# Kernel optimization log

Hardware: AMD Instinct MI355X
Metric: run time of the kernel (lower is better)

## Reference

```python
import jax, jax.numpy as jnp
import numpy as np

B, P, K = 8, 1024, 20          # clouds, points per cloud, knn neighbors
H, HD = 256, 512               # module hidden_dim, edge-MLP hidden (TransformerBlockRes default)
L, C = 3, 512                  # n_hidden_layers, n_components
N = B * P
LN_EPS = 1e-5


def _layer_norm(x, g, b):
    m = jnp.mean(x, axis=-1, keepdims=True)
    v = jnp.var(x, axis=-1, keepdims=True)
    return (x - m) * jax.lax.rsqrt(v + LN_EPS) * g + b


def _mlp(x, W1, b1, g1, be1, W2, b2, g2, be2):
    # Linear -> LayerNorm -> ELU -> Linear -> LayerNorm -> ELU (pos_nn / attn_nn)
    h = jax.nn.elu(_layer_norm(x @ W1 + b1, g1, be1))
    return jax.nn.elu(_layer_norm(h @ W2 + b2, g2, be2))


def _knn(pos):
    # knn_graph within each cloud, loop=False (self excluded). Equal-size clouds.
    p = pos.reshape(B, P, 3)
    d2 = jnp.sum((p[:, :, None, :] - p[:, None, :, :]) ** 2, axis=-1)  # [B,P,P]
    d2 = d2 + jnp.eye(P, dtype=d2.dtype) * 1e10                        # exclude self
    idx = jax.lax.top_k(-d2, K)[1]                                     # [B,P,K]
    return (idx + (jnp.arange(B) * P)[:, None, None]).reshape(N, K)    # global ids


def setup_inputs() -> dict:
    key = jax.random.key(0)
    cnt = [0]

    def nrm(shape, scale):
        cnt[0] += 1
        return (jax.random.normal(jax.random.fold_in(key, cnt[0]), shape, dtype=jnp.float32) * scale)

    d = {}
    d["pos"] = nrm((N, 3), 1.0)
    d["batch"] = jnp.repeat(jnp.arange(B, dtype=jnp.int32), P)
    # stem Linear(3, H)
    d["ffm_W"] = nrm((3, H), 3 ** -0.5); d["ffm_b"] = jnp.zeros((H,), jnp.float32)
    # PointTransformerConv linears (no bias), stacked over L layers
    s = H ** -0.5
    d["lin_W"] = nrm((L, H, H), s); d["src_W"] = nrm((L, H, H), s); d["dst_W"] = nrm((L, H, H), s)
    # pos_nn: Linear(3,HD)+LN+ELU+Linear(HD,H)+LN+ELU
    d["pos1_W"] = nrm((L, 3, HD), 3 ** -0.5); d["pos1_b"] = jnp.zeros((L, HD), jnp.float32)
    d["pos_ln1_g"] = jnp.ones((L, HD), jnp.float32); d["pos_ln1_b"] = jnp.zeros((L, HD), jnp.float32)
    d["pos2_W"] = nrm((L, HD, H), HD ** -0.5); d["pos2_b"] = jnp.zeros((L, H), jnp.float32)
    d["pos_ln2_g"] = jnp.ones((L, H), jnp.float32); d["pos_ln2_b"] = jnp.zeros((L, H), jnp.float32)
    # attn_nn: Linear(H,HD)+LN+ELU+Linear(HD,H)+LN+ELU
    d["att1_W"] = nrm((L, H, HD), s); d["att1_b"] = jnp.zeros((L, HD), jnp.float32)
    d["att_ln1_g"] = jnp.ones((L, HD), jnp.float32); d["att_ln1_b"] = jnp.zeros((L, HD), jnp.float32)
    d["att2_W"] = nrm((L, HD, H), HD ** -0.5); d["att2_b"] = jnp.zeros((L, H), jnp.float32)
    d["att_ln2_g"] = jnp.ones((L, H), jnp.float32); d["att_ln2_b"] = jnp.zeros((L, H), jnp.float32)
    # per-layer tail: LayerNorm + ELU + Linear + ResidualCoefficient
    d["blk_ln_g"] = jnp.ones((L, H), jnp.float32); d["blk_ln_b"] = jnp.zeros((L, H), jnp.float32)
    d["blk_W"] = nrm((L, H, H), s); d["blk_b"] = jnp.zeros((L, H), jnp.float32)
    d["res_alpha"] = nrm((L,), 0.1)  # torch init is zeros; small random for a nontrivial test
    d["r1_W"] = nrm((H, H), s); d["r1_b"] = jnp.zeros((H,), jnp.float32)
    d["r2_W"] = nrm((H, H), s); d["r2_b"] = jnp.zeros((H,), jnp.float32)
    d["r2_ln_g"] = jnp.ones((H,), jnp.float32); d["r2_ln_b"] = jnp.zeros((H,), jnp.float32)
    d["r3_W"] = nrm((H, H), s); d["r3_b"] = jnp.zeros((H,), jnp.float32)
    d["r3_ln_g"] = jnp.ones((H,), jnp.float32); d["r3_ln_b"] = jnp.zeros((H,), jnp.float32)
    d["r4_W"] = nrm((H, C), s); d["r4_b"] = jnp.zeros((C,), jnp.float32)
    return d


def reference(pos, batch, ffm_W, ffm_b, lin_W, src_W, dst_W,
              pos1_W, pos1_b, pos_ln1_g, pos_ln1_b, pos2_W, pos2_b, pos_ln2_g, pos_ln2_b,
              att1_W, att1_b, att_ln1_g, att_ln1_b, att2_W, att2_b, att_ln2_g, att_ln2_b,
              blk_ln_g, blk_ln_b, blk_W, blk_b, res_alpha,
              r1_W, r1_b, r2_W, r2_b, r2_ln_g, r2_ln_b, r3_W, r3_b, r3_ln_g, r3_ln_b, r4_W, r4_b):
    # knn graph is identical every layer (pos never changes) -> compute once
    neigh = _knn(pos)                       # [N,K] neighbor (source) ids j for each target i
    rel = pos[:, None, :] - pos[neigh]      # pos_i - pos_j, [N,K,3]
    x = pos @ ffm_W + ffm_b                 # [N,H]
    for i in range(L):
        a_src = x @ src_W[i]                # [N,H]
        a_dst = x @ dst_W[i]
        v = x @ lin_W[i]
        delta = _mlp(rel, pos1_W[i], pos1_b[i], pos_ln1_g[i], pos_ln1_b[i],
                     pos2_W[i], pos2_b[i], pos_ln2_g[i], pos_ln2_b[i])          # [N,K,H]
        alpha = _mlp(a_dst[:, None, :] - a_src[neigh] + delta,
                     att1_W[i], att1_b[i], att_ln1_g[i], att_ln1_b[i],
                     att2_W[i], att2_b[i], att_ln2_g[i], att_ln2_b[i])          # [N,K,H]
        attn = jax.nn.softmax(alpha, axis=1)                                    # per-channel over K neighbors
        agg = jnp.sum(attn * (v[neigh] + delta), axis=1)                        # sum aggregation (PyG default)
        h = jax.nn.elu(_layer_norm(agg, blk_ln_g[i], blk_ln_b[i])) @ blk_W[i] + blk_b[i]
        x = x + res_alpha[i] * h
    h = x @ r1_W + r1_b                                                         # [N,H]
    pooled = jax.ops.segment_max(h, batch, num_segments=B)                      # global_max_pool [B,H]
    h = jax.nn.elu(_layer_norm(pooled @ r2_W + r2_b, r2_ln_g, r2_ln_b))
    h = jax.nn.elu(_layer_norm(h @ r3_W + r3_b, r3_ln_g, r3_ln_b))
    return h @ r4_W + r4_b                                                      # [B,C]
```

## Files before the change

### kernel.cpp

```cpp
#include <hip/hip_runtime.h>
#include <math.h>

#define NPTS 8192
#define PPC  1024
#define BCL  8
#define KNN  20
#define HDIM 256
#define HD2  512
#define NL   3
#define NCOMP 512
#define EDG  (NPTS*KNN)
#define QS   768

typedef __bf16 bf16x8 __attribute__((ext_vector_type(8)));
typedef float f32x4 __attribute__((ext_vector_type(4)));
typedef unsigned int uint4v __attribute__((ext_vector_type(4)));
typedef unsigned short us8 __attribute__((ext_vector_type(8)));

__device__ inline unsigned short f2bf(float f) {
  unsigned u = __float_as_uint(f);
  u += 0x7FFF + ((u >> 16) & 1);
  return (unsigned short)(u >> 16);
}
__device__ inline unsigned short f2bf_fast(float f) {
  return (unsigned short)((__float_as_uint(f) + 0x8000u) >> 16);
}
__device__ inline unsigned pack2bf(float a, float b) {
  return ((__float_as_uint(a) + 0x8000u) >> 16) |
         ((__float_as_uint(b) + 0x8000u) & 0xFFFF0000u);
}
__device__ inline float bf2f(unsigned short u) {
  return __uint_as_float((unsigned)u << 16);
}
__device__ inline float elu(float y) { return (y > 0.f) ? y : (__expf(y) - 1.f); }

__global__ __launch_bounds__(256)
void knn_wave(const float* __restrict__ pos, int* __restrict__ neigh,
              float* __restrict__ rel_f) {
  __shared__ float px[PPC], py[PPC], pz[PPC];
  int tid = threadIdx.x;
  int i0 = blockIdx.x * 4;
  int base = i0 & ~(PPC - 1);
  for (int t = tid; t < PPC; t += 256) {
    px[t] = pos[(size_t)(base + t) * 3 + 0];
    py[t] = pos[(size_t)(base + t) * 3 + 1];
    pz[t] = pos[(size_t)(base + t) * 3 + 2];
  }
  __syncthreads();
  int wave = tid >> 6, lane = tid & 63;
  int i = i0 + wave;
  int il = i - base;
  float xi = px[il], yi = py[il], zi = pz[il];
  float d[16];
  #pragma unroll
  for (int q = 0; q < 16; ++q) {
    int t = lane + 64 * q;
    float dx = xi - px[t], dy = yi - py[t], dz = zi - pz[t];
    float dd = dx * dx + dy * dy + dz * dz;
    d[q] = (t == il) ? 3.4e38f : dd;
  }
  int mywin = 0;
  for (int k = 0; k < KNN; ++k) {
    float v = d[0]; int idx = lane;
    #pragma unroll
    for (int q = 1; q < 16; ++q)
      if (d[q] < v) { v = d[q]; idx = q * 64 + lane; }
    #pragma unroll
    for (int off = 1; off < 64; off <<= 1) {
      float ov = __shfl_xor(v, off, 64);
      int oi = __shfl_xor(idx, off, 64);
      if (ov < v || (ov == v && oi < idx)) { v = ov; idx = oi; }
    }
    if (lane == k) mywin = idx;
    int qwin = idx >> 6;
    bool own = (idx & 63) == lane;
    #pragma unroll
    for (int q = 0; q < 16; ++q)
      if (own && q == qwin) d[q] = 3.4e38f;
  }
  if (lane < KNN) {
    neigh[(size_t)i * KNN + lane] = base + mywin;
    size_t rb = ((size_t)i * KNN + lane) * 3;
    rel_f[rb + 0] = xi - px[mywin];
    rel_f[rb + 1] = yi - py[mywin];
    rel_f[rb + 2] = zi - pz[mywin];
  }
}

__global__ __launch_bounds__(256)
void transpose_w(const float* __restrict__ W, unsigned short* __restrict__ out,
                 int K, int N, int Kpad) {
  int n = blockIdx.x;
  for (int k = threadIdx.x; k < Kpad; k += 256)
    out[(size_t)n * Kpad + k] = (k < K) ? f2bf(W[(size_t)k * N + n]) : (unsigned short)0;
}

__global__ __launch_bounds__(64)
void pack_w(const float* __restrict__ W, unsigned short* __restrict__ out, int N) {
  int blk = blockIdx.x;
  int NT = N / 16;
  int ks = blk / NT, nt = blk % NT;
  int lane = threadIdx.x;
  int l16 = lane & 15, quad = lane >> 4;
  int col = nt * 16 + l16;
  int krow = ks * 32 + quad * 8;
  unsigned short o[8];
  #pragma unroll
  for (int j = 0; j < 8; ++j)
    o[j] = f2bf(W[(size_t)(krow + j) * N + col]);
  *(uint4v*)&out[((size_t)blk * 64 + lane) * 8] = *(uint4v*)o;
}

__global__ __launch_bounds__(256)
void prep_pos(const float* __restrict__ pos, unsigned short* __restrict__ posb) {
  int idx = blockIdx.x * 256 + threadIdx.x;
  int m = idx >> 5, c = idx & 31;
  posb[idx] = (c < 3) ? f2bf(pos[(size_t)m * 3 + c]) : (unsigned short)0;
}

__global__ __launch_bounds__(256, 3)
void pos_fused(const float* __restrict__ rel_f, const float* __restrict__ W1,
               const float* __restrict__ b1, const float* __restrict__ g1,
               const float* __restrict__ be1,
               const unsigned short* __restrict__ B2p, const float* __restrict__ bias2,
               const float* __restrict__ g2, const float* __restrict__ be2,
               unsigned short* __restrict__ delta_b, int edge_base) {
  __shared__ alignas(16) char smem[46976];
  unsigned short* H = (unsigned short*)smem;
  float* w1s = (float*)(smem + 33280);
  float* b1s = w1s + 1536;
  float* g1s = b1s + 512;
  float* be1s = g1s + 512;
  float* lnsum = (float*)(smem + 45568);
  float* lnsq  = (float*)(smem + 46080);
  float* relS  = (float*)(smem + 46592);
  int tid = threadIdx.x;
  int wave = tid >> 6, lane = tid & 63;
  int el0 = blockIdx.x * 32;
  int eg0 = edge_base + el0;
  for (int t = tid; t < 1536; t += 256) w1s[t] = W1[t];
  for (int t = tid; t < 512; t += 256) { b1s[t] = b1[t]; g1s[t] = g1[t]; be1s[t] = be1[t]; }
  if (tid < 96) relS[tid] = rel_f[(size_t)eg0 * 3 + tid];
  __syncthreads();
  {
    int rIW = lane >> 3, sub = lane & 7;
    int row = wave * 8 + rIW;
    float r0 = relS[row * 3 + 0], r1v = relS[row * 3 + 1], r2v = relS[row * 3 + 2];
    int cb = sub * 64;
    float h[64]; float s = 0.f, sq = 0.f;
    #pragma unroll
    for (int cc = 0; cc < 16; ++cc) {
      f32x4 w0 = *(const f32x4*)&w1s[cb + cc * 4];
      f32x4 wa = *(const f32x4*)&w1s[512 + cb + cc * 4];
      f32x4 wb = *(const f32x4*)&w1s[1024 + cb + cc * 4];
      f32x4 bb = *(const f32x4*)&b1s[cb + cc * 4];
      #pragma unroll
      for (int q = 0; q < 4; ++q) {
        float hv = fmaf(r0, w0[q], fmaf(r1v, wa[q], fmaf(r2v, wb[q], bb[q])));
        h[cc * 4 + q] = hv; s += hv; sq += hv * hv;
      }
    }
    #pragma unroll
    for (int off = 1; off < 8; off <<= 1) { s += __shfl_xor(s, off, 64); sq += __shfl_xor(sq, off, 64); }
    float mean = s * (1.f / 512.f);
    float var = sq * (1.f / 512.f) - mean * mean;
    float rr = rsqrtf(var + 1e-5f);
    #pragma unroll
    for (int cc = 0; cc < 8; ++cc) {
      unsigned u[4];
      #pragma unroll
      for (int q = 0; q < 4; ++q) {
        int c0 = cb + cc * 8 + 2 * q;
        float y0 = elu((h[cc * 8 + 2 * q]     - mean) * rr * g1s[c0]     + be1s[c0]);
        float y1 = elu((h[cc * 8 + 2 * q + 1] - mean) * rr * g1s[c0 + 1] + be1s[c0 + 1]);
        u[q] = pack2bf(y0, y1);
      }
      *(uint4v*)&H[row * 520 + cb + cc * 8] = *(uint4v*)u;
    }
  }
  __syncthreads();
  int quad = lane >> 4, l16 = lane & 15;
  int cb2 = wave * 64;
  f32x4 acc2[2][4] = {};
  #pragma unroll 4
  for (int ks = 0; ks < 16; ++ks) {
    bf16x8 bvv[4];
    #pragma unroll
    for (int ni = 0; ni < 4; ++ni)
      bvv[ni] = *(const bf16x8*)(B2p + ((size_t)(ks * 16 + wave * 4 + ni) * 64 + lane) * 8);
    bf16x8 a0 = __builtin_bit_cast(bf16x8, *(const uint4v*)&H[(l16) * 520 + ks * 32 + quad * 8]);
    bf16x8 a1 = __builtin_bit_cast(bf16x8, *(const uint4v*)&H[(16 + l16) * 520 + ks * 32 + quad * 8]);
    #pragma unroll
    for (int ni = 0; ni < 4; ++ni) {
      acc2[0][ni] = __builtin_amdgcn_mfma_f32_16x16x32_bf16(a0, bvv[ni], acc2[0][ni], 0, 0, 0);
      acc2[1][ni] = __builtin_amdgcn_mfma_f32_16x16x32_bf16(a1, bvv[ni], acc2[1][ni], 0, 0, 0);
    }
  }
  float b2v[4], g2v[4], be2v[4];
  #pragma unroll
  for (int ni = 0; ni < 4; ++ni) {
    int col = cb2 + ni * 16 + l16;
    b2v[ni] = bias2[col]; g2v[ni] = g2[col]; be2v[ni] = be2[col];
  }
  #pragma unroll
  for (int mt = 0; mt < 2; ++mt)
    #pragma unroll
    for (int r = 0; r < 4; ++r) {
      int row = mt * 16 + quad * 4 + r;
      float s2 = 0.f, q2 = 0.f;
      #pragma unroll
      for (int ni = 0; ni < 4; ++ni) {
        float val = acc2[mt][ni][r] + b2v[ni];
        acc2[mt][ni][r] = val; s2 += val; q2 += val * val;
      }
      #pragma unroll
      for (int off = 1; off < 16; off <<= 1) { s2 += __shfl_xor(s2, off, 64); q2 += __shfl_xor(q2, off, 64); }
      if (l16 == 0) { lnsum[wave * 32 + row] = s2; lnsq[wave * 32 + row] = q2; }
    }
  __syncthreads();
  #pragma unroll
  for (int mt = 0; mt < 2; ++mt)
    #pragma unroll
    for (int r = 0; r < 4; ++r) {
      int row = mt * 16 + quad * 4 + r;
      float tot = lnsum[row] + lnsum[32 + row] + lnsum[64 + row] + lnsum[96 + row];
      float tsq = lnsq[row] + lnsq[32 + row] + lnsq[64 + row] + lnsq[96 + row];
      float mean = tot * (1.f / 256.f);
      float var = tsq * (1.f / 256.f) - mean * mean;
      float rr = rsqrtf(var + 1e-5f);
      size_t ob = (size_t)(el0 + row) * 256;
      #pragma unroll
      for (int ni = 0; ni < 4; ++ni)
        delta_b[ob + cb2 + ni * 16 + l16] =
            f2bf_fast(elu((acc2[mt][ni][r] - mean) * rr * g2v[ni] + be2v[ni]));
    }
}

__global__ __launch_bounds__(256, 3)
void attn_fused(const unsigned short* __restrict__ qkv,
                const unsigned short* __restrict__ delta_b,
                const int* __restrict__ neigh,
                const unsigned short* __restrict__ B1p, const float* __restrict__ bias1,
                const float* __restrict__ g1, const float* __restrict__ be1,
                const unsigned short* __restrict__ B2p, const float* __restrict__ bias2,
                const float* __restrict__ g2, const float* __restrict__ be2,
                unsigned short* __restrict__ alpha_b, int edge_base) {
  __shared__ alignas(16) char smem[34560];
  unsigned short* As = (unsigned short*)smem;
  unsigned short* H  = (unsigned short*)smem;
  float* lnsum = (float*)(smem + 33280);
  float* lnsq  = (float*)(smem + 33792);
  int* iS = (int*)(smem + 34304);
  int* jS = (int*)(smem + 34432);
  int tid = threadIdx.x;
  int wave = tid >> 6, lane = tid & 63;
  int quad = lane >> 4, l16 = lane & 15;
  int el0 = blockIdx.x * 32;
  int eg0 = edge_base + el0;
  if (tid < 32) { iS[tid] = (eg0 + tid) / KNN; jS[tid] = neigh[eg0 + tid]; }
  __syncthreads();
  {
    int r = tid & 31, seg = tid >> 5;
    int i = iS[r], j = jS[r], e = el0 + r;
    int c0 = seg * 32;
    #pragma unroll
    for (int q4 = 0; q4 < 4; ++q4) {
      int c = c0 + q4 * 8;
      us8 pd = *(const us8*)(qkv + (size_t)i * QS + 256 + c);
      us8 ps = *(const us8*)(qkv + (size_t)j * QS + c);
      us8 pl = *(const us8*)(delta_b + (size_t)e * 256 + c);
      unsigned u[4];
      #pragma unroll
      for (int q = 0; q < 4; ++q)
        u[q] = pack2bf(bf2f(pd[2*q])   - bf2f(ps[2*q])   + bf2f(pl[2*q]),
                       bf2f(pd[2*q+1]) - bf2f(ps[2*q+1]) + bf2f(pl[2*q+1]));
      *(uint4v*)&As[r * 264 + c] = *(uint4v*)u;
    }
  }
  __syncthreads();
  int cb1 = wave * 128;
  f32x4 acc1[2][8] = {};
  #pragma unroll 2
  for (int ks = 0; ks < 8; ++ks) {
    bf16x8 a0 = __builtin_bit_cast(bf16x8, *(const uint4v*)&As[(l16) * 264 + ks * 32 + quad * 8]);
    bf16x8 a1 = __builtin_bit_cast(bf16x8, *(const uint4v*)&As[(16 + l16) * 264 + ks * 32 + quad * 8]);
    #pragma unroll
    for (int half = 0; half < 2; ++half) {
      bf16x8 bvv[4];
      #pragma unroll
      for (int ni = 0; ni < 4; ++ni)
        bvv[ni] = *(const bf16x8*)(B1p + ((size_t)(ks * 32 + wave * 8 + half * 4 + ni) * 64 + lane) * 8);
      #pragma unroll
      for (int ni = 0; ni < 4; ++ni) {
        acc1[0][half * 4 + ni] = __builtin_amdgcn_mfma_f32_16x16x32_bf16(a0, bvv[ni], acc1[0][half * 4 + ni], 0, 0, 0);
        acc1[1][half * 4 + ni] = __builtin_amdgcn_mfma_f32_16x16x32_bf16(a1, bvv[ni], acc1[1][half * 4 + ni], 0, 0, 0);
      }
    }
  }
  {
    #pragma unroll
    for (int mt = 0; mt < 2; ++mt)
      #pragma unroll
      for (int r = 0; r < 4; ++r) {
        int row = mt * 16 + quad * 4 + r;
        float s = 0.f, sq = 0.f;
        #pragma unroll
        for (int ni = 0; ni < 8; ++ni) {
          float val = acc1[mt][ni][r] + bias1[cb1 + ni * 16 + l16];
          acc1[mt][ni][r] = val; s += val; sq += val * val;
        }
        #pragma unroll
        for (int off = 1; off < 16; off <<= 1) { s += __shfl_xor(s, off, 64); sq += __shfl_xor(sq, off, 64); }
        if (l16 == 0) { lnsum[wave * 32 + row] = s; lnsq[wave * 32 + row] = sq; }
      }
    __syncthreads();
    #pragma unroll
    for (int mt = 0; mt < 2; ++mt)
      #pragma unroll
      for (int r = 0; r < 4; ++r) {
        int row = mt * 16 + quad * 4 + r;
        float tot = lnsum[row] + lnsum[32 + row] + lnsum[64 + row] + lnsum[96 + row];
        float tsq = lnsq[row] + lnsq[32 + row] + lnsq[64 + row] + lnsq[96 + row];
        float mean = tot * (1.f / 512.f);
        float var = tsq * (1.f / 512.f) - mean * mean;
        float rr = rsqrtf(var + 1e-5f);
        #pragma unroll
        for (int ni = 0; ni < 8; ++ni) {
          int col = cb1 + ni * 16 + l16;
          H[row * 520 + col] = f2bf_fast(elu((acc1[mt][ni][r] - mean) * rr * g1[col] + be1[col]));
        }
      }
  }
  __syncthreads();
  int cb2 = wave * 64;
  f32x4 acc2[2][4] = {};
  #pragma unroll 4
  for (int ks = 0; ks < 16; ++ks) {
    bf16x8 bvv[4];
    #pragma unroll
    for (int ni = 0; ni < 4; ++ni)
      bvv[ni] = *(const bf16x8*)(B2p + ((size_t)(ks * 16 + wave * 4 + ni) * 64 + lane) * 8);
    bf16x8 a0 = __builtin_bit_cast(bf16x8, *(const uint4v*)&H[(l16) * 520 + ks * 32 + quad * 8]);
    bf16x8 a1 = __builtin_bit_cast(bf16x8, *(const uint4v*)&H[(16 + l16) * 520 + ks * 32 + quad * 8]);
    #pragma unroll
    for (int ni = 0; ni < 4; ++ni) {
      acc2[0][ni] = __builtin_amdgcn_mfma_f32_16x16x32_bf16(a0, bvv[ni], acc2[0][ni], 0, 0, 0);
      acc2[1][ni] = __builtin_amdgcn_mfma_f32_16x16x32_bf16(a1, bvv[ni], acc2[1][ni], 0, 0, 0);
    }
  }
  float b2v[4], g2v[4], be2v[4];
  #pragma unroll
  for (int ni = 0; ni < 4; ++ni) {
    int col = cb2 + ni * 16 + l16;
    b2v[ni] = bias2[col]; g2v[ni] = g2[col]; be2v[ni] = be2[col];
  }
  #pragma unroll
  for (int mt = 0; mt < 2; ++mt)
    #pragma unroll
    for (int r = 0; r < 4; ++r) {
      int row = mt * 16 + quad * 4 + r;
      float s2 = 0.f, q2 = 0.f;
      #pragma unroll
      for (int ni = 0; ni < 4; ++ni) {
        float val = acc2[mt][ni][r] + b2v[ni];
        acc2[mt][ni][r] = val; s2 += val; q2 += val * val;
      }
      #pragma unroll
      for (int off = 1; off < 16; off <<= 1) { s2 += __shfl_xor(s2, off, 64); q2 += __shfl_xor(q2, off, 64); }
      if (l16 == 0) { lnsum[wave * 32 + row] = s2; lnsq[wave * 32 + row] = q2; }
    }
  __syncthreads();
  #pragma unroll
  for (int mt = 0; mt < 2; ++mt)
    #pragma unroll
    for (int r = 0; r < 4; ++r) {
      int row = mt * 16 + quad * 4 + r;
      float tot = lnsum[row] + lnsum[32 + row] + lnsum[64 + row] + lnsum[96 + row];
      float tsq = lnsq[row] + lnsq[32 + row] + lnsq[64 + row] + lnsq[96 + row];
      float mean = tot * (1.f / 256.f);
      float var = tsq * (1.f / 256.f) - mean * mean;
      float rr = rsqrtf(var + 1e-5f);
      size_t ob = (size_t)(el0 + row) * 256;
      #pragma unroll
      for (int ni = 0; ni < 4; ++ni)
        alpha_b[ob + cb2 + ni * 16 + l16] =
            f2bf_fast(elu((acc2[mt][ni][r] - mean) * rr * g2v[ni] + be2v[ni]));
    }
}

#define APAD 40
__global__ __launch_bounds__(256)
void gemm_mfma(const unsigned short* __restrict__ A, const unsigned short* __restrict__ Bt,
               const float* __restrict__ bias, float* __restrict__ Cf,
               unsigned short* __restrict__ Cb, int M, int Nn, int Kk) {
  __shared__ alignas(16) unsigned short As[128 * APAD];
  __shared__ alignas(16) unsigned short Bs[128 * APAD];
  int tid = threadIdx.x;
  int wave = tid >> 6, lane = tid & 63;
  int quad = lane >> 4, l16 = lane & 15;
  int wm = (wave >> 1) * 64, wn = (wave & 1) * 64;
  int m0 = blockIdx.y * 128, n0 = blockIdx.x * 128;
  f32x4 acc[4][4] = {};
  int srow = tid >> 2;
  int scol = (tid & 3) * 8;
  for (int k0 = 0; k0 < Kk; k0 += 32) {
    #pragma unroll
    for (int h = 0; h < 2; ++h) {
      int r = srow + h * 64;
      int gm = m0 + r;
      uint4v va = {0, 0, 0, 0};
      if (gm < M) va = *(const uint4v*)(A + (size_t)gm * Kk + k0 + scol);
      *(uint4v*)(&As[r * APAD + scol]) = va;
      int gn = n0 + r;
      uint4v vb = *(const uint4v*)(Bt + (size_t)gn * Kk + k0 + scol);
      *(uint4v*)(&Bs[r * APAD + scol]) = vb;
    }
    __syncthreads();
    bf16x8 af[4], bfr[4];
    #pragma unroll
    for (int mi = 0; mi < 4; ++mi)
      af[mi] = __builtin_bit_cast(bf16x8, *(const uint4v*)(&As[(wm + mi * 16 + l16) * APAD + quad * 8]));
    #pragma unroll
    for (int ni = 0; ni < 4; ++ni)
      bfr[ni] = __builtin_bit_cast(bf16x8, *(const uint4v*)(&Bs[(wn + ni * 16 + l16) * APAD + quad * 8]));
    #pragma unroll
    for (int mi = 0; mi < 4; ++mi)
      #pragma unroll
      for (int ni = 0; ni < 4; ++ni)
        acc[mi][ni] = __builtin_amdgcn_mfma_f32_16x16x32_bf16(af[mi], bfr[ni], acc[mi][ni], 0, 0, 0);
    __syncthreads();
  }
  float bvs[4]; int gns[4];
  #pragma unroll
  for (int ni = 0; ni < 4; ++ni) {
    gns[ni] = n0 + wn + ni * 16 + l16;
    bvs[ni] = bias ? bias[gns[ni]] : 0.f;
  }
  #pragma unroll
  for (int mi = 0; mi < 4; ++mi) {
    #pragma unroll
    for (int r = 0; r < 4; ++r) {
      int gm = m0 + wm + mi * 16 + quad * 4 + r;
      if (gm >= M) continue;
      #pragma unroll
      for (int ni = 0; ni < 4; ++ni) {
        float val = acc[mi][ni][r] + bvs[ni];
        if (Cf) Cf[(size_t)gm * Nn + gns[ni]] = val;
        if (Cb) Cb[(size_t)gm * Nn + gns[ni]] = f2bf_fast(val);
      }
    }
  }
}

#define BM0 64
#define BN0 64
#define BK0 16
__global__ __launch_bounds__(256)
void gemm_bias(const float* __restrict__ A, const float* __restrict__ Bw,
               const float* __restrict__ bias, float* __restrict__ C,
               int M, int Nn, int Kk) {
  __shared__ float Asm[BK0][BM0 + 1];
  __shared__ float Bsm[BK0][BN0 + 1];
  int bm = blockIdx.y * BM0, bn = blockIdx.x * BN0;
  int tid = threadIdx.x;
  int tx = tid & 15, ty = tid >> 4;
  float acc[4][4] = {{0.f}};
  for (int k0 = 0; k0 < Kk; k0 += BK0) {
    #pragma unroll
    for (int ii = 0; ii < 4; ++ii) {
      int e = tid + ii * 256;
      int m = e >> 4, k = e & 15;
      int gm = bm + m, gk = k0 + k;
      Asm[k][m] = (gm < M && gk < Kk) ? A[(size_t)gm * Kk + gk] : 0.f;
    }
    #pragma unroll
    for (int ii = 0; ii < 4; ++ii) {
      int e = tid + ii * 256;
      int k = e >> 6, n = e & 63;
      int gk = k0 + k, gn = bn + n;
      Bsm[k][n] = (gk < Kk && gn < Nn) ? Bw[(size_t)gk * Nn + gn] : 0.f;
    }
    __syncthreads();
    #pragma unroll
    for (int kk = 0; kk < BK0; ++kk) {
      float a[4], b[4];
      #pragma unroll
      for (int ii = 0; ii < 4; ++ii) a[ii] = Asm[kk][ty * 4 + ii];
      #pragma unroll
      for (int jj = 0; jj < 4; ++jj) b[jj] = Bsm[kk][tx * 4 + jj];
      #pragma unroll
      for (int ii = 0; ii < 4; ++ii)
        #pragma unroll
        for (int jj = 0; jj < 4; ++jj)
          acc[ii][jj] += a[ii] * b[jj];
    }
    __syncthreads();
  }
  #pragma unroll
  for (int ii = 0; ii < 4; ++ii) {
    int gm = bm + ty * 4 + ii;
    if (gm >= M) continue;
    #pragma unroll
    for (int jj = 0; jj < 4; ++jj) {
      int gn = bn + tx * 4 + jj;
      if (gn >= Nn) continue;
      float vv = acc[ii][jj];
      if (bias) vv += bias[gn];
      C[(size_t)gm * Nn + gn] = vv;
    }
  }
}

__global__ __launch_bounds__(256)
void ln_elu_kernel(const float* __restrict__ in, float* __restrict__ outf,
                   unsigned short* __restrict__ outb,
                   const float* __restrict__ g, const float* __restrict__ bb,
                   int Cn, int do_elu) {
  __shared__ float sdata[4];
  size_t row = blockIdx.x;
  const float* x = in + row * Cn;
  int tid = threadIdx.x;
  float v0 = x[tid];
  float v1 = (Cn == 512) ? x[tid + 256] : 0.f;
  float s = v0 + v1;
  #pragma unroll
  for (int off = 32; off > 0; off >>= 1) s += __shfl_xor(s, off, 64);
  if ((tid & 63) == 0) sdata[tid >> 6] = s;
  __syncthreads();
  float mean = (sdata[0] + sdata[1] + sdata[2] + sdata[3]) / (float)Cn;
  float d0 = v0 - mean;
  float d1 = (Cn == 512) ? (v1 - mean) : 0.f;
  float sq = d0 * d0 + d1 * d1;
  __syncthreads();
  #pragma unroll
  for (int off = 32; off > 0; off >>= 1) sq += __shfl_xor(sq, off, 64);
  if ((tid & 63) == 0) sdata[tid >> 6] = sq;
  __syncthreads();
  float var = (sdata[0] + sdata[1] + sdata[2] + sdata[3]) / (float)Cn;
  float r = rsqrtf(var + 1e-5f);
  float y0 = d0 * r * g[tid] + bb[tid];
  if (do_elu) y0 = elu(y0);
  if (outf) outf[row * Cn + tid] = y0;
  if (outb) outb[row * Cn + tid] = f2bf_fast(y0);
  if (Cn == 512) {
    float y1 = d1 * r * g[tid + 256] + bb[tid + 256];
    if (do_elu) y1 = elu(y1);
    if (outf) outf[row * Cn + tid + 256] = y1;
    if (outb) outb[row * Cn + tid + 256] = f2bf_fast(y1);
  }
}

__global__ __launch_bounds__(256)
void softmax_agg(const unsigned short* __restrict__ alpha_b,
                 const unsigned short* __restrict__ delta_b,
                 const unsigned short* __restrict__ qkv,
                 const int* __restrict__ neigh,
                 float* __restrict__ agg, int node0) {
  int nl = blockIdx.x;
  int c = threadIdx.x;
  int i = node0 + nl;
  float av[KNN];
  float mx = -3.4e38f;
  #pragma unroll
  for (int k = 0; k < KNN; ++k) {
    av[k] = bf2f(alpha_b[((size_t)nl * KNN + k) * HDIM + c]);
    mx = fmaxf(mx, av[k]);
  }
  float ssum = 0.f;
  #pragma unroll
  for (int k = 0; k < KNN; ++k) { av[k] = __expf(av[k] - mx); ssum += av[k]; }
  float inv = 1.f / ssum;
  float acc = 0.f;
  #pragma unroll
  for (int k = 0; k < KNN; ++k) {
    int j = neigh[(size_t)i * KNN + k];
    acc += av[k] * inv * (bf2f(qkv[(size_t)j * QS + 512 + c]) +
                          bf2f(delta_b[((size_t)nl * KNN + k) * HDIM + c]));
  }
  agg[(size_t)i * HDIM + c] = acc;
}

__global__ __launch_bounds__(256)
void axpy_res(float* __restrict__ x, unsigned short* __restrict__ xb,
              const float* __restrict__ h, const float* __restrict__ alpha, int l) {
  size_t idx = (size_t)blockIdx.x * 256 + threadIdx.x;
  float nv = x[idx] + alpha[l] * h[idx];
  x[idx] = nv;
  xb[idx] = f2bf_fast(nv);
}

__global__ __launch_bounds__(256)
void seg_max_p(const float* __restrict__ h, float* __restrict__ part) {
  int blk = blockIdx.x;
  int b = blk >> 4, ch = blk & 15;
  int c = threadIdx.x;
  const float* base = h + ((size_t)b * PPC + (size_t)ch * 64) * HDIM;
  float m = -3.4e38f;
  for (int p = 0; p < 64; ++p)
    m = fmaxf(m, base[(size_t)p * HDIM + c]);
  part[(size_t)blk * HDIM + c] = m;
}
__global__ __launch_bounds__(256)
void seg_max_f(const float* __restrict__ part, float* __restrict__ pooled) {
  int b = blockIdx.x;
  int c = threadIdx.x;
  float m = -3.4e38f;
  for (int k = 0; k < 16; ++k)
    m = fmaxf(m, part[(size_t)(b * 16 + k) * HDIM + c]);
  pooled[(size_t)b * HDIM + c] = m;
}

extern "C" void kernel_launch(void* const* d_in, const int* in_sizes, int n_in,
                              void* d_out, int out_size, void* d_ws, size_t ws_size,
                              hipStream_t stream) {
  const float* pos       = (const float*)d_in[0];
  const float* ffm_W     = (const float*)d_in[2];
  const float* ffm_b     = (const float*)d_in[3];
  const float* lin_W     = (const float*)d_in[4];
  const float* src_W     = (const float*)d_in[5];
  const float* dst_W     = (const float*)d_in[6];
  const float* pos1_W    = (const float*)d_in[7];
  const float* pos1_b    = (const float*)d_in[8];
  const float* pos_ln1_g = (const float*)d_in[9];
  const float* pos_ln1_b = (const float*)d_in[10];
  const float* pos2_W    = (const float*)d_in[11];
  const float* pos2_b    = (const float*)d_in[12];
  const float* pos_ln2_g = (const float*)d_in[13];
  const float* pos_ln2_b = (const float*)d_in[14];
  const float* att1_W    = (const float*)d_in[15];
  const float* att1_b    = (const float*)d_in[16];
  const float* att_ln1_g = (const float*)d_in[17];
  const float* att_ln1_b = (const float*)d_in[18];
  const float* att2_W    = (const float*)d_in[19];
  const float* att2_b    = (const float*)d_in[20];
  const float* att_ln2_g = (const float*)d_in[21];
  const float* att_ln2_b = (const float*)d_in[22];
  const float* blk_ln_g  = (const float*)d_in[23];
  const float* blk_ln_b  = (const float*)d_in[24];
  const float* blk_W     = (const float*)d_in[25];
  const float* blk_b     = (const float*)d_in[26];
  const float* res_alpha = (const float*)d_in[27];
  const float* r1_W = (const float*)d_in[28]; const float* r1_b = (const float*)d_in[29];
  const float* r2_W = (const float*)d_in[30]; const float* r2_b = (const float*)d_in[31];
  const float* r2_ln_g = (const float*)d_in[32]; const float* r2_ln_b = (const float*)d_in[33];
  const float* r3_W = (const float*)d_in[34]; const float* r3_b = (const float*)d_in[35];
  const float* r3_ln_g = (const float*)d_in[36]; const float* r3_ln_b = (const float*)d_in[37];
  const float* r4_W = (const float*)d_in[38]; const float* r4_b = (const float*)d_in[39];
  float* out = (float*)d_out;

  char* wsp = (char*)d_ws;
  auto alloc = [&](size_t bytes) -> void* {
    void* p = (void*)wsp;
    wsp += (bytes + 255) & ~(size_t)255;
    return p;
  };
  int*            neigh   = (int*)alloc(EDG * sizeof(int));
  float*          rel_f   = (float*)alloc((size_t)EDG * 3 * 4);
  unsigned short* posb    = (unsigned short*)alloc((size_t)NPTS * 32 * 2);
  float*          x       = (float*)alloc((size_t)NPTS * HDIM * 4);
  unsigned short* xb      = (unsigned short*)alloc((size_t)NPTS * HDIM * 2);
  unsigned short* xln_b   = (unsigned short*)alloc((size_t)NPTS * HDIM * 2);
  unsigned short* qkv     = (unsigned short*)alloc((size_t)NPTS * QS * 2);
  float*          agg     = (float*)alloc((size_t)NPTS * HDIM * 4);
  float*          segp    = (float*)alloc((size_t)128 * HDIM * 4);
  float*          pooled  = (float*)alloc((size_t)BCL * HDIM * 4);
  float*          hh      = (float*)alloc((size_t)BCL * HDIM * 4);
  unsigned short* ffmt = (unsigned short*)alloc((size_t)HDIM * 32 * 2);
  unsigned short* r1t  = (unsigned short*)alloc((size_t)HDIM * HDIM * 2);
  unsigned short *qkvt[NL], *blkt[NL];
  unsigned short *pos2p[NL], *att1p[NL], *att2p[NL];
  for (int l = 0; l < NL; ++l) {
    qkvt[l]  = (unsigned short*)alloc((size_t)QS * HDIM * 2);
    blkt[l]  = (unsigned short*)alloc((size_t)HDIM * HDIM * 2);
    pos2p[l] = (unsigned short*)alloc((size_t)HDIM * HD2 * 2);
    att1p[l] = (unsigned short*)alloc((size_t)HD2 * HDIM * 2);
    att2p[l] = (unsigned short*)alloc((size_t)HDIM * HD2 * 2);
  }
  size_t used = (size_t)(wsp - (char*)d_ws);
  size_t avail = (ws_size > used) ? (ws_size - used) : 0;
  size_t per_node = (size_t)KNN * (HDIM * 2 * 2) + 1024;
  int Nc = (int)(avail / per_node);
  if (Nc > NPTS) Nc = NPTS;
  Nc &= ~15;
  if (Nc < 16) Nc = 16;
  unsigned short* delta_b = (unsigned short*)alloc((size_t)Nc * KNN * HDIM * 2);
  unsigned short* alpha_b = (unsigned short*)alloc((size_t)Nc * KNN * HDIM * 2);

  auto mgemm = [&](const unsigned short* A, const unsigned short* Bt, const float* bias,
                   float* Cf, unsigned short* Cb, int M, int Nn, int Kk) {
    dim3 g(Nn / 128, (M + 127) / 128);
    gemm_mfma<<<g, dim3(256), 0, stream>>>(A, Bt, bias, Cf, Cb, M, Nn, Kk);
  };
  auto fgemm = [&](const float* A, const float* Bw, const float* bias, float* Cp,
                   int M, int Nn, int Kk) {
    dim3 g((Nn + BN0 - 1) / BN0, (M + BM0 - 1) / BM0);
    gemm_bias<<<g, dim3(256), 0, stream>>>(A, Bw, bias, Cp, M, Nn, Kk);
  };

  transpose_w<<<HDIM, 256, 0, stream>>>(ffm_W, ffmt, 3, HDIM, 32);
  transpose_w<<<HDIM, 256, 0, stream>>>(r1_W, r1t, HDIM, HDIM, HDIM);
  for (int l = 0; l < NL; ++l) {
    transpose_w<<<HDIM, 256, 0, stream>>>(src_W + (size_t)l * HDIM * HDIM, qkvt[l], HDIM, HDIM, HDIM);
    transpose_w<<<HDIM, 256, 0, stream>>>(dst_W + (size_t)l * HDIM * HDIM, qkvt[l] + 256 * 256, HDIM, HDIM, HDIM);
    transpose_w<<<HDIM, 256, 0, stream>>>(lin_W + (size_t)l * HDIM * HDIM, qkvt[l] + 512 * 256, HDIM, HDIM, HDIM);
    transpose_w<<<HDIM, 256, 0, stream>>>(blk_W + (size_t)l * HDIM * HDIM, blkt[l], HDIM, HDIM, HDIM);
    pack_w<<<(HD2 / 32) * (HDIM / 16), 64, 0, stream>>>(pos2_W + (size_t)l * HD2 * HDIM, pos2p[l], HDIM);
    pack_w<<<(HDIM / 32) * (HD2 / 16), 64, 0, stream>>>(att1_W + (size_t)l * HDIM * HD2, att1p[l], HD2);
    pack_w<<<(HD2 / 32) * (HDIM / 16), 64, 0, stream>>>(att2_W + (size_t)l * HD2 * HDIM, att2p[l], HDIM);
  }

  knn_wave<<<NPTS / 4, 256, 0, stream>>>(pos, neigh, rel_f);
  prep_pos<<<NPTS * 32 / 256, 256, 0, stream>>>(pos, posb);
  mgemm(posb, ffmt, ffm_b, x, xb, NPTS, HDIM, 32);

  for (int l = 0; l < NL; ++l) {
    mgemm(xb, qkvt[l], nullptr, nullptr, qkv, NPTS, QS, HDIM);

    for (int n0 = 0; n0 < NPTS; n0 += Nc) {
      int nc = (Nc < NPTS - n0) ? Nc : (NPTS - n0);
      int ec = nc * KNN;
      pos_fused<<<ec / 32, 256, 0, stream>>>(
          rel_f, pos1_W + (size_t)l * 3 * HD2, pos1_b + (size_t)l * HD2,
          pos_ln1_g + (size_t)l * HD2, pos_ln1_b + (size_t)l * HD2,
          pos2p[l], pos2_b + (size_t)l * HDIM,
          pos_ln2_g + (size_t)l * HDIM, pos_ln2_b + (size_t)l * HDIM,
          delta_b, n0 * KNN);
      attn_fused<<<ec / 32, 256, 0, stream>>>(
          qkv, delta_b, neigh,
          att1p[l], att1_b + (size_t)l * HD2,
          att_ln1_g + (size_t)l * HD2, att_ln1_b + (size_t)l * HD2,
          att2p[l], att2_b + (size_t)l * HDIM,
          att_ln2_g + (size_t)l * HDIM, att_ln2_b + (size_t)l * HDIM,
          alpha_b, n0 * KNN);
      softmax_agg<<<nc, 256, 0, stream>>>(alpha_b, delta_b, qkv, neigh, agg, n0);
    }
    ln_elu_kernel<<<NPTS, 256, 0, stream>>>(agg, nullptr, xln_b,
                                            blk_ln_g + (size_t)l * HDIM, blk_ln_b + (size_t)l * HDIM, HDIM, 1);
    mgemm(xln_b, blkt[l], blk_b + (size_t)l * HDIM, agg, nullptr, NPTS, HDIM, HDIM);
    axpy_res<<<(NPTS * HDIM) / 256, 256, 0, stream>>>(x, xb, agg, res_alpha, l);
  }

  mgemm(xb, r1t, r1_b, agg, nullptr, NPTS, HDIM, HDIM);
  seg_max_p<<<128, 256, 0, stream>>>(agg, segp);
  seg_max_f<<<BCL, 256, 0, stream>>>(segp, pooled);
  fgemm(pooled, r2_W, r2_b, hh, BCL, HDIM, HDIM);
  ln_elu_kernel<<<BCL, 256, 0, stream>>>(hh, hh, nullptr, r2_ln_g, r2_ln_b, HDIM, 1);
  fgemm(hh, r3_W, r3_b, pooled, BCL, HDIM, HDIM);
  ln_elu_kernel<<<BCL, 256, 0, stream>>>(pooled, pooled, nullptr, r3_ln_g, r3_ln_b, HDIM, 1);
  fgemm(pooled, r4_W, r4_b, out, BCL, NCOMP, HDIM);
}
```

Measured before the change: 1.962 ms.

## Enlarge attn_fused tile to 64 edges with 8 waves per block

attn_fused now processes 64 edges per block using 512 threads (8 waves). Each wave covers a narrower column slice across four 16-row M tiles, so every weight fragment loaded from global memory feeds twice as many rows and total weight traffic per edge is halved. Shared memory grows to about 70 KB per block and the LayerNorm partial sums are now reduced across 8 waves. The occupancy hint of 3 is also dropped from pos_fused and attn_fused, which may change register allocation and the number of resident waves.

```diff
diff --git a/kernel.cpp b/kernel.cpp
--- a/kernel.cpp
+++ b/kernel.cpp
@@ -118,7 +118,7 @@
   posb[idx] = (c < 3) ? f2bf(pos[(size_t)m * 3 + c]) : (unsigned short)0;
 }
 
-__global__ __launch_bounds__(256, 3)
+__global__ __launch_bounds__(256)
 void pos_fused(const float* __restrict__ rel_f, const float* __restrict__ W1,
                const float* __restrict__ b1, const float* __restrict__ g1,
                const float* __restrict__ be1,
@@ -236,7 +236,7 @@
     }
 }
 
-__global__ __launch_bounds__(256, 3)
+__global__ __launch_bounds__(512)
 void attn_fused(const unsigned short* __restrict__ qkv,
                 const unsigned short* __restrict__ delta_b,
                 const int* __restrict__ neigh,
@@ -245,22 +245,22 @@
                 const unsigned short* __restrict__ B2p, const float* __restrict__ bias2,
                 const float* __restrict__ g2, const float* __restrict__ be2,
                 unsigned short* __restrict__ alpha_b, int edge_base) {
-  __shared__ alignas(16) char smem[34560];
+  __shared__ alignas(16) char smem[71168];
   unsigned short* As = (unsigned short*)smem;
   unsigned short* H  = (unsigned short*)smem;
-  float* lnsum = (float*)(smem + 33280);
-  float* lnsq  = (float*)(smem + 33792);
-  int* iS = (int*)(smem + 34304);
-  int* jS = (int*)(smem + 34432);
+  float* lnsum = (float*)(smem + 66560);
+  float* lnsq  = (float*)(smem + 68608);
+  int* iS = (int*)(smem + 70656);
+  int* jS = (int*)(smem + 70912);
   int tid = threadIdx.x;
   int wave = tid >> 6, lane = tid & 63;
   int quad = lane >> 4, l16 = lane & 15;
-  int el0 = blockIdx.x * 32;
+  int el0 = blockIdx.x * 64;
   int eg0 = edge_base + el0;
-  if (tid < 32) { iS[tid] = (eg0 + tid) / KNN; jS[tid] = neigh[eg0 + tid]; }
+  if (tid < 64) { iS[tid] = (eg0 + tid) / KNN; jS[tid] = neigh[eg0 + tid]; }
   __syncthreads();
   {
-    int r = tid & 31, seg = tid >> 5;
+    int r = tid & 63, seg = tid >> 6;
     int i = iS[r], j = jS[r], e = el0 + r;
     int c0 = seg * 32;
     #pragma unroll
@@ -278,111 +278,114 @@
     }
   }
   __syncthreads();
-  int cb1 = wave * 128;
-  f32x4 acc1[2][8] = {};
+  int cb1 = wave * 64;
+  f32x4 acc1[4][4] = {};
   #pragma unroll 2
   for (int ks = 0; ks < 8; ++ks) {
-    bf16x8 a0 = __builtin_bit_cast(bf16x8, *(const uint4v*)&As[(l16) * 264 + ks * 32 + quad * 8]);
-    bf16x8 a1 = __builtin_bit_cast(bf16x8, *(const uint4v*)&As[(16 + l16) * 264 + ks * 32 + quad * 8]);
-    #pragma unroll
-    for (int half = 0; half < 2; ++half) {
-      bf16x8 bvv[4];
+    bf16x8 bvv[4];
+    #pragma unroll
+    for (int ni = 0; ni < 4; ++ni)
+      bvv[ni] = *(const bf16x8*)(B1p + ((size_t)(ks * 32 + wave * 4 + ni) * 64 + lane) * 8);
+    bf16x8 a[4];
+    #pragma unroll
+    for (int mt = 0; mt < 4; ++mt)
+      a[mt] = __builtin_bit_cast(bf16x8, *(const uint4v*)&As[(mt * 16 + l16) * 264 + ks * 32 + quad * 8]);
+    #pragma unroll
+    for (int mt = 0; mt < 4; ++mt)
       #pragma unroll
       for (int ni = 0; ni < 4; ++ni)
-        bvv[ni] = *(const bf16x8*)(B1p + ((size_t)(ks * 32 + wave * 8 + half * 4 + ni) * 64 + lane) * 8);
-      #pragma unroll
-      for (int ni = 0; ni < 4; ++ni) {
-        acc1[0][half * 4 + ni] = __builtin_amdgcn_mfma_f32_16x16x32_bf16(a0, bvv[ni], acc1[0][half * 4 + ni], 0, 0, 0);
-        acc1[1][half * 4 + ni] = __builtin_amdgcn_mfma_f32_16x16x32_bf16(a1, bvv[ni], acc1[1][half * 4 + ni], 0, 0, 0);
-      }
-    }
+        acc1[mt][ni] = __builtin_amdgcn_mfma_f32_16x16x32_bf16(a[mt], bvv[ni], acc1[mt][ni], 0, 0, 0);
   }
   {
     #pragma unroll
-    for (int mt = 0; mt < 2; ++mt)
+    for (int mt = 0; mt < 4; ++mt)
       #pragma unroll
       for (int r = 0; r < 4; ++r) {
         int row = mt * 16 + quad * 4 + r;
         float s = 0.f, sq = 0.f;
         #pragma unroll
-        for (int ni = 0; ni < 8; ++ni) {
+        for (int ni = 0; ni < 4; ++ni) {
           float val = acc1[mt][ni][r] + bias1[cb1 + ni * 16 + l16];
           acc1[mt][ni][r] = val; s += val; sq += val * val;
         }
         #pragma unroll
         for (int off = 1; off < 16; off <<= 1) { s += __shfl_xor(s, off, 64); sq += __shfl_xor(sq, off, 64); }
-        if (l16 == 0) { lnsum[wave * 32 + row] = s; lnsq[wave * 32 + row] = sq; }
+        if (l16 == 0) { lnsum[wave * 64 + row] = s; lnsq[wave * 64 + row] = sq; }
       }
     __syncthreads();
     #pragma unroll
-    for (int mt = 0; mt < 2; ++mt)
+    for (int mt = 0; mt < 4; ++mt)
       #pragma unroll
       for (int r = 0; r < 4; ++r) {
         int row = mt * 16 + quad * 4 + r;
-        float tot = lnsum[row] + lnsum[32 + row] + lnsum[64 + row] + lnsum[96 + row];
-        float tsq = lnsq[row] + lnsq[32 + row] + lnsq[64 + row] + lnsq[96 + row];
+        float tot = 0.f, tsq = 0.f;
+        #pragma unroll
+        for (int w = 0; w < 8; ++w) { tot += lnsum[w * 64 + row]; tsq += lnsq[w * 64 + row]; }
         float mean = tot * (1.f / 512.f);
         float var = tsq * (1.f / 512.f) - mean * mean;
         float rr = rsqrtf(var + 1e-5f);
         #pragma unroll
-        for (int ni = 0; ni < 8; ++ni) {
+        for (int ni = 0; ni < 4; ++ni) {
           int col = cb1 + ni * 16 + l16;
           H[row * 520 + col] = f2bf_fast(elu((acc1[mt][ni][r] - mean) * rr * g1[col] + be1[col]));
         }
       }
   }
   __syncthreads();
-  int cb2 = wave * 64;
-  f32x4 acc2[2][4] = {};
-  #pragma unroll 4
+  int cb2 = wave * 32;
+  f32x4 acc2[4][2] = {};
+  #pragma unroll 2
   for (int ks = 0; ks < 16; ++ks) {
-    bf16x8 bvv[4];
-    #pragma unroll
-    for (int ni = 0; ni < 4; ++ni)
-      bvv[ni] = *(const bf16x8*)(B2p + ((size_t)(ks * 16 + wave * 4 + ni) * 64 + lane) * 8);
-    bf16x8 a0 = __builtin_bit_cast(bf16x8, *(const uint4v*)&H[(l16) * 520 + ks * 32 + quad * 8]);
-    bf16x8 a1 = __builtin_bit_cast(bf16x8, *(const uint4v*)&H[(16 + l16) * 520 + ks * 32 + quad * 8]);
-    #pragma unroll
-    for (int ni = 0; ni < 4; ++ni) {
-      acc2[0][ni] = __builtin_amdgcn_mfma_f32_16x16x32_bf16(a0, bvv[ni], acc2[0][ni], 0, 0, 0);
-      acc2[1][ni] = __builtin_amdgcn_mfma_f32_16x16x32_bf16(a1, bvv[ni], acc2[1][ni], 0, 0, 0);
-    }
-  }
-  float b2v[4], g2v[4], be2v[4];
-  #pragma unroll
-  for (int ni = 0; ni < 4; ++ni) {
+    bf16x8 bvv[2];
+    #pragma unroll
+    for (int ni = 0; ni < 2; ++ni)
+      bvv[ni] = *(const bf16x8*)(B2p + ((size_t)(ks * 16 + wave * 2 + ni) * 64 + lane) * 8);
+    bf16x8 a[4];
+    #pragma unroll
+    for (int mt = 0; mt < 4; ++mt)
+      a[mt] = __builtin_bit_cast(bf16x8, *(const uint4v*)&H[(mt * 16 + l16) * 520 + ks * 32 + quad * 8]);
+    #pragma unroll
+    for (int mt = 0; mt < 4; ++mt)
+      #pragma unroll
+      for (int ni = 0; ni < 2; ++ni)
+        acc2[mt][ni] = __builtin_amdgcn_mfma_f32_16x16x32_bf16(a[mt], bvv[ni], acc2[mt][ni], 0, 0, 0);
+  }
+  float b2v[2], g2v[2], be2v[2];
+  #pragma unroll
+  for (int ni = 0; ni < 2; ++ni) {
     int col = cb2 + ni * 16 + l16;
     b2v[ni] = bias2[col]; g2v[ni] = g2[col]; be2v[ni] = be2[col];
   }
   #pragma unroll
-  for (int mt = 0; mt < 2; ++mt)
+  for (int mt = 0; mt < 4; ++mt)
     #pragma unroll
     for (int r = 0; r < 4; ++r) {
       int row = mt * 16 + quad * 4 + r;
       float s2 = 0.f, q2 = 0.f;
       #pragma unroll
-      for (int ni = 0; ni < 4; ++ni) {
+      for (int ni = 0; ni < 2; ++ni) {
         float val = acc2[mt][ni][r] + b2v[ni];
         acc2[mt][ni][r] = val; s2 += val; q2 += val * val;
       }
       #pragma unroll
       for (int off = 1; off < 16; off <<= 1) { s2 += __shfl_xor(s2, off, 64); q2 += __shfl_xor(q2, off, 64); }
-      if (l16 == 0) { lnsum[wave * 32 + row] = s2; lnsq[wave * 32 + row] = q2; }
-    }
-  __syncthreads();
-  #pragma unroll
-  for (int mt = 0; mt < 2; ++mt)
+      if (l16 == 0) { lnsum[wave * 64 + row] = s2; lnsq[wave * 64 + row] = q2; }
+    }
+  __syncthreads();
+  #pragma unroll
+  for (int mt = 0; mt < 4; ++mt)
     #pragma unroll
     for (int r = 0; r < 4; ++r) {
       int row = mt * 16 + quad * 4 + r;
-      float tot = lnsum[row] + lnsum[32 + row] + lnsum[64 + row] + lnsum[96 + row];
-      float tsq = lnsq[row] + lnsq[32 + row] + lnsq[64 + row] + lnsq[96 + row];
+      float tot = 0.f, tsq = 0.f;
+      #pragma unroll
+      for (int w = 0; w < 8; ++w) { tot += lnsum[w * 64 + row]; tsq += lnsq[w * 64 + row]; }
       float mean = tot * (1.f / 256.f);
       float var = tsq * (1.f / 256.f) - mean * mean;
       float rr = rsqrtf(var + 1e-5f);
       size_t ob = (size_t)(el0 + row) * 256;
       #pragma unroll
-      for (int ni = 0; ni < 4; ++ni)
+      for (int ni = 0; ni < 2; ++ni)
         alpha_b[ob + cb2 + ni * 16 + l16] =
             f2bf_fast(elu((acc2[mt][ni][r] - mean) * rr * g2v[ni] + be2v[ni]));
     }
@@ -725,7 +728,7 @@
           pos2p[l], pos2_b + (size_t)l * HDIM,
           pos_ln2_g + (size_t)l * HDIM, pos_ln2_b + (size_t)l * HDIM,
           delta_b, n0 * KNN);
-      attn_fused<<<ec / 32, 256, 0, stream>>>(
+      attn_fused<<<ec / 64, 512, 0, stream>>>(
           qkv, delta_b, neigh,
           att1p[l], att1_b + (size_t)l * HD2,
           att_ln1_g + (size_t)l * HD2, att_ln1_b + (size_t)l * HD2,
```

Result: slower. 2.025 ms (+3.2%).
